# Performance work log

Hardware: AMD Instinct MI355X
Metric: run time of the kernel (lower is better)

Reference implementation:

```python
import jax, jax.numpy as jnp
import numpy as np

G, N, C, R, NCOMP, F = 1, 2097152, 16, 320, 48, 27


def _interp_plane(src, u, v):
    # src: (G, C, H, W). Torch grid_sample convention: u (grid x) indexes W (last dim),
    # v (grid y) indexes H. align_corners=True, bilinear, zero padding. Returns (G, N, C).
    _, _, H, W = src.shape
    x = (u + 1.0) * 0.5 * (W - 1)
    y = (v + 1.0) * 0.5 * (H - 1)
    x0 = jnp.floor(x)
    y0 = jnp.floor(y)
    wx = x - x0
    wy = y - y0
    x0i = x0.astype(jnp.int32)
    y0i = y0.astype(jnp.int32)

    def corner(xi, yi, w):
        inb = ((xi >= 0) & (xi < W) & (yi >= 0) & (yi < H)).astype(src.dtype)
        xc = jnp.clip(xi, 0, W - 1)
        yc = jnp.clip(yi, 0, H - 1)
        vals = jax.vmap(lambda s, yy, xx: s[:, yy, xx])(src, yc, xc)  # (G, C, N)
        return vals * (w * inb)[:, None, :]

    out = (corner(x0i, y0i, (1.0 - wx) * (1.0 - wy))
           + corner(x0i + 1, y0i, wx * (1.0 - wy))
           + corner(x0i, y0i + 1, (1.0 - wx) * wy)
           + corner(x0i + 1, y0i + 1, wx * wy))
    return out.transpose(0, 2, 1)  # (G, N, C)


def _interp_line(src, t):
    # src: (G, C, L), t in [-1, 1]. 1D linear interp, align_corners=True, zero padding.
    _, _, L = src.shape
    x = (t + 1.0) * 0.5 * (L - 1)
    x0 = jnp.floor(x)
    wx = x - x0
    x0i = x0.astype(jnp.int32)

    def corner(xi, w):
        inb = ((xi >= 0) & (xi < L)).astype(src.dtype)
        xc = jnp.clip(xi, 0, L - 1)
        vals = jax.vmap(lambda s, xx: s[:, xx])(src, xc)  # (G, C, N)
        return vals * (w * inb)[:, None, :]

    out = corner(x0i, 1.0 - wx) + corner(x0i + 1, wx)
    return out.transpose(0, 2, 1)  # (G, N, C)


def setup_inputs() -> dict:
    key = jax.random.key(0)
    ks = jax.random.split(key, 8)
    return {
        "points": jax.random.uniform(ks[0], (G, N, 3), jnp.float32, minval=-1.0, maxval=1.0),
        "matrix_components_xy": jax.random.normal(ks[1], (G, C, R, R), jnp.float32) * 0.1,
        "matrix_components_yz": jax.random.normal(ks[2], (G, C, R, R), jnp.float32) * 0.1,
        "matrix_components_xz": jax.random.normal(ks[3], (G, C, R, R), jnp.float32) * 0.1,
        "vector_components_x": jax.random.normal(ks[4], (G, C, R), jnp.float32) * 0.1,
        "vector_components_y": jax.random.normal(ks[5], (G, C, R), jnp.float32) * 0.1,
        "vector_components_z": jax.random.normal(ks[6], (G, C, R), jnp.float32) * 0.1,
        "basis_matrix": jax.random.normal(ks[7], (G, NCOMP, F), jnp.float32) * 0.1,
    }


def reference(points, matrix_components_xy, matrix_components_yz, matrix_components_xz,
              vector_components_x, vector_components_y, vector_components_z, basis_matrix):
    recorded_shape = points.shape
    p = points.reshape(points.shape[0], -1, points.shape[-1])  # (G, N, 3)
    px, py, pz = p[..., 0], p[..., 1], p[..., 2]
    # points[..., :2] -> grid x = px (indexes W of xy plane), grid y = py
    a = _interp_plane(matrix_components_xy, px, py) * _interp_line(vector_components_z, pz)
    # points[..., [0, 2]] -> grid x = px, grid y = pz
    b = _interp_plane(matrix_components_xz, px, pz) * _interp_line(vector_components_y, py)
    # points[..., 1:] -> grid x = py, grid y = pz
    c = _interp_plane(matrix_components_yz, py, pz) * _interp_line(vector_components_x, px)
    feats = jnp.concatenate((a, b, c), axis=-1)  # (G, N, 3C)
    result = jnp.einsum('gnc,gcf->gnf', feats, basis_matrix)  # (G, N, F)
    return result.reshape(*recorded_shape[:-1], -1)
```

## Files before the change

kernel.cpp:

```cpp
#include <hip/hip_runtime.h>
#include <hip/hip_fp16.h>
#include <stdint.h>


constexpr int NPTS = 2097152;
constexpr int CCH  = 16;
constexpr int RES  = 320;
constexpr long long HW = (long long)RES * RES;
constexpr int FD   = 27;
constexpr int BLK  = 256;
constexpr int NCELL = 512;
constexpr int PTS_PER_SORTBLK = 4096;

constexpr int HIST_BLOCKS = NPTS / PTS_PER_SORTBLK;
constexpr int PLANE_BLOCKS = 1200;
constexpr int LINE_BLOCKS = 4;

constexpr size_t WS_PLANEH = 0;
constexpr size_t WS_LINEH  = WS_PLANEH + 3ull*HW*CCH*2;
constexpr size_t WS_BFRAG  = WS_LINEH + 3ull*RES*CCH*2;
constexpr size_t WS_CHIST  = WS_BFRAG + 3072;
constexpr size_t WS_CURSOR = WS_CHIST + (size_t)NCELL*4;
constexpr size_t WS_SORTED = WS_CURSOR + (size_t)NCELL*4;
constexpr size_t WS_NEED   = WS_SORTED + (size_t)NPTS*16;

typedef _Float16 half8 __attribute__((ext_vector_type(8)));
typedef float f32x16 __attribute__((ext_vector_type(16)));

__device__ __forceinline__ unsigned spread3(unsigned v) {
    return (v & 1u) | ((v & 2u) << 2) | ((v & 4u) << 4);
}
__device__ __forceinline__ int cell_key8(float px, float py, float pz) {
    int cx = min(max((int)((px + 1.f) * 4.f), 0), 7);
    int cy = min(max((int)((py + 1.f) * 4.f), 0), 7);
    int cz = min(max((int)((pz + 1.f) * 4.f), 0), 7);
    return (int)(spread3((unsigned)cx) | (spread3((unsigned)cy) << 1) | (spread3((unsigned)cz) << 2));
}

__global__ __launch_bounds__(BLK) void prep_kernel(
    const float* __restrict__ pts,
    const float* __restrict__ pxy, const float* __restrict__ pxz, const float* __restrict__ pyz,
    const float* __restrict__ vx, const float* __restrict__ vy, const float* __restrict__ vz,
    const float* __restrict__ basis,
    __half* __restrict__ planesH, __half* __restrict__ linesH, __half* __restrict__ bfragH,
    unsigned* __restrict__ chist) {
    __shared__ unsigned lh[NCELL];
    const int bid = blockIdx.x;
    const int tid = threadIdx.x;
    if (bid < HIST_BLOCKS) {
        lh[tid] = 0u; lh[tid + 256] = 0u;
        __syncthreads();
        const float4* p4 = ((const float4*)pts) + (size_t)bid * 3072;
        #pragma unroll
        for (int g = 0; g < 4; ++g) {
            const float4 a = p4[tid*12 + g*3 + 0];
            const float4 b = p4[tid*12 + g*3 + 1];
            const float4 c = p4[tid*12 + g*3 + 2];
            atomicAdd(&lh[cell_key8(a.x, a.y, a.z)], 1u);
            atomicAdd(&lh[cell_key8(a.w, b.x, b.y)], 1u);
            atomicAdd(&lh[cell_key8(b.z, b.w, c.x)], 1u);
            atomicAdd(&lh[cell_key8(c.y, c.z, c.w)], 1u);
        }
        __syncthreads();
        if (lh[tid])       atomicAdd(&chist[tid],       lh[tid]);
        if (lh[tid + 256]) atomicAdd(&chist[tid + 256], lh[tid + 256]);
    } else if (bid < HIST_BLOCKS + PLANE_BLOCKS) {
        const int pb = bid - HIST_BLOCKS;
        const int plane = pb / 400;
        const int texel = (pb % 400) * BLK + tid;
        const float* src = (plane == 0) ? pxy : (plane == 1 ? pxz : pyz);
        union { ushort u[16]; uint4 q[2]; } pk;
        #pragma unroll
        for (int c = 0; c < CCH; ++c)
            pk.u[c] = __half_as_ushort(__float2half(src[(size_t)c * HW + texel]));
        uint4* dst = (uint4*)(planesH + ((size_t)plane * HW + texel) * CCH);
        dst[0] = pk.q[0]; dst[1] = pk.q[1];
    } else if (bid < HIST_BLOCKS + PLANE_BLOCKS + LINE_BLOCKS) {
        const int idx = (bid - HIST_BLOCKS - PLANE_BLOCKS) * BLK + tid;
        if (idx >= 3 * RES) return;
        const int axis = idx / RES, t = idx % RES;
        const float* src = (axis == 0) ? vx : (axis == 1 ? vy : vz);
        union { ushort u[16]; uint4 q[2]; } pk;
        #pragma unroll
        for (int c = 0; c < CCH; ++c)
            pk.u[c] = __half_as_ushort(__float2half(src[c * RES + t]));
        uint4* dst = (uint4*)(linesH + ((size_t)axis * RES + t) * CCH);
        dst[0] = pk.q[0]; dst[1] = pk.q[1];
    } else {
        if (tid < 192) {
            const int r = tid >> 6, l = tid & 63;
            const int col = l & 31, kb = l >> 5;
            __half* dst = bfragH + tid * 8;
            #pragma unroll
            for (int j = 0; j < 8; ++j) {
                float v = (col < FD) ? basis[(r * 16 + kb * 8 + j) * FD + col] : 0.f;
                dst[j] = __float2half(v);
            }
        }
    }
}

__global__ __launch_bounds__(NCELL) void scan_kernel(const unsigned* __restrict__ chist,
                                                     unsigned* __restrict__ cursor) {
    __shared__ unsigned l[NCELL];
    const int t = threadIdx.x;
    const unsigned v = chist[t];
    l[t] = v;
    __syncthreads();
    for (int o = 1; o < NCELL; o <<= 1) {
        unsigned u = (t >= o) ? l[t - o] : 0u;
        __syncthreads();
        l[t] += u;
        __syncthreads();
    }
    cursor[t] = l[t] - v;
}

__global__ __launch_bounds__(BLK) void scatter_kernel(const float* __restrict__ pts,
                                                      unsigned* __restrict__ cursor,
                                                      float4* __restrict__ sorted) {
    __shared__ unsigned lh[NCELL];
    __shared__ unsigned lb[NCELL];
    const int bid = blockIdx.x;
    const int tid = threadIdx.x;
    lh[tid] = 0u; lh[tid + 256] = 0u;
    __syncthreads();
    const float4* p4 = ((const float4*)pts) + (size_t)bid * 3072;
    unsigned kr[16];
    #pragma unroll
    for (int g = 0; g < 4; ++g) {
        const float4 a = p4[tid*12 + g*3 + 0];
        const float4 b = p4[tid*12 + g*3 + 1];
        const float4 c = p4[tid*12 + g*3 + 2];
        int k; unsigned r;
        k = cell_key8(a.x, a.y, a.z); r = atomicAdd(&lh[k], 1u); kr[g*4+0] = ((unsigned)k << 16) | r;
        k = cell_key8(a.w, b.x, b.y); r = atomicAdd(&lh[k], 1u); kr[g*4+1] = ((unsigned)k << 16) | r;
        k = cell_key8(b.z, b.w, c.x); r = atomicAdd(&lh[k], 1u); kr[g*4+2] = ((unsigned)k << 16) | r;
        k = cell_key8(c.y, c.z, c.w); r = atomicAdd(&lh[k], 1u); kr[g*4+3] = ((unsigned)k << 16) | r;
    }
    __syncthreads();
    lb[tid]       = atomicAdd(&cursor[tid],       lh[tid]);
    lb[tid + 256] = atomicAdd(&cursor[tid + 256], lh[tid + 256]);
    __syncthreads();
    const int ibase = bid * PTS_PER_SORTBLK + tid * 16;
    #pragma unroll
    for (int g = 0; g < 4; ++g) {
        const float4 a = p4[tid*12 + g*3 + 0];
        const float4 b = p4[tid*12 + g*3 + 1];
        const float4 c = p4[tid*12 + g*3 + 2];
        unsigned e;
        e = kr[g*4+0]; sorted[lb[e >> 16] + (e & 0xffffu)] = make_float4(a.x, a.y, a.z, __int_as_float(ibase + g*4 + 0));
        e = kr[g*4+1]; sorted[lb[e >> 16] + (e & 0xffffu)] = make_float4(a.w, b.x, b.y, __int_as_float(ibase + g*4 + 1));
        e = kr[g*4+2]; sorted[lb[e >> 16] + (e & 0xffffu)] = make_float4(b.z, b.w, c.x, __int_as_float(ibase + g*4 + 2));
        e = kr[g*4+3]; sorted[lb[e >> 16] + (e & 0xffffu)] = make_float4(c.y, c.z, c.w, __int_as_float(ibase + g*4 + 3));
    }
}

__device__ __forceinline__ half8 interp8h(const uint4* __restrict__ P, const uint4* __restrict__ L,
                                          int t00, int t01, int t10, int t11, int l0, int l1,
                                          float wc, float wr, float lw, int h) {
    union U { uint4 u; __half2 h2[4]; half8 v; };
    U c00, c01, c10, c11, la, lb, res;
    c00.u = P[2*t00 + h]; c01.u = P[2*t01 + h];
    c10.u = P[2*t10 + h]; c11.u = P[2*t11 + h];
    la.u  = L[2*l0 + h];  lb.u  = L[2*l1 + h];
    const float w00 = (1.f - wc) * (1.f - wr), w01 = wc * (1.f - wr);
    const float w10 = (1.f - wc) * wr,         w11 = wc * wr;
    const __half2 w00h = __float2half2_rn(w00), w01h = __float2half2_rn(w01);
    const __half2 w10h = __float2half2_rn(w10), w11h = __float2half2_rn(w11);
    const __half2 lwh  = __float2half2_rn(lw),  mlwh = __float2half2_rn(1.f - lw);
    #pragma unroll
    for (int q = 0; q < 4; ++q) {
        __half2 s = __hmul2(c00.h2[q], w00h);
        s = __hfma2(c01.h2[q], w01h, s);
        s = __hfma2(c10.h2[q], w10h, s);
        s = __hfma2(c11.h2[q], w11h, s);
        __half2 l = __hmul2(la.h2[q], mlwh);
        l = __hfma2(lb.h2[q], lwh, l);
        res.h2[q] = __hmul2(s, l);
    }
    return res.v;
}

__global__ __launch_bounds__(BLK) void eval_kernel(
    const float4* __restrict__ sorted,
    const __half* __restrict__ planesH,
    const __half* __restrict__ linesH,
    const __half* __restrict__ bfragH,
    float* __restrict__ out) {
    __shared__ int s_oi[BLK];
    constexpr int NBLK = NPTS / BLK;
    constexpr int CHUNK = NBLK / 8;
    const int bid = blockIdx.x;
    const int tid = threadIdx.x;
    const int swz = (bid & 7) * CHUNK + (bid >> 3);
    const int wid = tid >> 6, lane = tid & 63;
    const int pcol = lane & 31, kb = lane >> 5;

    union BU { uint4 u; half8 h; } b0u, b1u, b2u;
    const uint4* bf = (const uint4*)bfragH;
    b0u.u = bf[lane]; b1u.u = bf[64 + lane]; b2u.u = bf[128 + lane];

    const uint4* Pxy = (const uint4*)planesH;
    const uint4* Pxz = (const uint4*)(planesH + (size_t)HW * CCH);
    const uint4* Pyz = (const uint4*)(planesH + (size_t)2 * HW * CCH);
    const uint4* Lx = (const uint4*)linesH;
    const uint4* Ly = (const uint4*)(linesH + (size_t)RES * CCH);
    const uint4* Lz = (const uint4*)(linesH + (size_t)2 * RES * CCH);

    const int blockbase = swz * BLK;
    #pragma unroll
    for (int t = 0; t < 2; ++t) {
        const int tbase = wid * 64 + t * 32;
        const float4 pt = sorted[blockbase + tbase + pcol];
        const float px = pt.x, py = pt.y, pz = pt.z;
        if (kb == 0) s_oi[tbase + pcol] = __float_as_int(pt.w);

        const float scl = 0.5f * (RES - 1);
        const float fx = (px + 1.f) * scl, fy = (py + 1.f) * scl, fz = (pz + 1.f) * scl;
        const float xf = floorf(fx), yf = floorf(fy), zf = floorf(fz);
        const float wx = fx - xf, wy = fy - yf, wz = fz - zf;
        int x0 = min(max((int)xf, 0), RES - 1);
        int y0 = min(max((int)yf, 0), RES - 1);
        int z0 = min(max((int)zf, 0), RES - 1);
        const int x1 = min(x0 + 1, RES - 1);
        const int y1 = min(y0 + 1, RES - 1);
        const int z1 = min(z0 + 1, RES - 1);

        f32x16 acc;
        #pragma unroll
        for (int r = 0; r < 16; ++r) acc[r] = 0.f;

        half8 a0 = interp8h(Pxy, Lz, y0*RES+x0, y0*RES+x1, y1*RES+x0, y1*RES+x1, z0, z1, wx, wy, wz, kb);
        acc = __builtin_amdgcn_mfma_f32_32x32x16_f16(a0, b0u.h, acc, 0, 0, 0);
        half8 a1 = interp8h(Pxz, Ly, z0*RES+x0, z0*RES+x1, z1*RES+x0, z1*RES+x1, y0, y1, wx, wz, wy, kb);
        acc = __builtin_amdgcn_mfma_f32_32x32x16_f16(a1, b1u.h, acc, 0, 0, 0);
        half8 a2 = interp8h(Pyz, Lx, z0*RES+y0, z0*RES+y1, z1*RES+y0, z1*RES+y1, x0, x1, wy, wz, wx, kb);
        acc = __builtin_amdgcn_mfma_f32_32x32x16_f16(a2, b2u.h, acc, 0, 0, 0);

        if (pcol < FD) {
            #pragma unroll
            for (int r = 0; r < 16; ++r) {
                const int row = (r & 3) + 8 * (r >> 2) + 4 * kb;
                const int o = s_oi[tbase + row];
                out[(size_t)o * FD + pcol] = acc[r];
            }
        }
    }
}

__device__ __forceinline__ float bilerp(const float* __restrict__ p,
                                        int o00, int o01, int o10, int o11,
                                        float wc, float wr) {
    float v00 = p[o00], v01 = p[o01], v10 = p[o10], v11 = p[o11];
    float top = v00 + wc * (v01 - v00);
    float bot = v10 + wc * (v11 - v10);
    return top + wr * (bot - top);
}

__global__ __launch_bounds__(BLK) void vm_eval_fallback(
    const float* __restrict__ pts,
    const float* __restrict__ pxy, const float* __restrict__ pyz, const float* __restrict__ pxz,
    const float* __restrict__ vx, const float* __restrict__ vy, const float* __restrict__ vz,
    const float* __restrict__ basis, float* __restrict__ out) {
    const long long i = (long long)blockIdx.x * BLK + threadIdx.x;
    const float px = pts[i*3], py = pts[i*3+1], pz = pts[i*3+2];
    const float scl = 0.5f * (RES - 1);
    const float fx = (px + 1.f) * scl, fy = (py + 1.f) * scl, fz = (pz + 1.f) * scl;
    const float xf = floorf(fx), yf = floorf(fy), zf = floorf(fz);
    const float wx = fx - xf, wy = fy - yf, wz = fz - zf;
    int x0 = min(max((int)xf, 0), RES - 1);
    int y0 = min(max((int)yf, 0), RES - 1);
    int z0 = min(max((int)zf, 0), RES - 1);
    const int x1 = min(x0+1, RES-1), y1 = min(y0+1, RES-1), z1 = min(z0+1, RES-1);
    float acc[FD];
    #pragma unroll
    for (int f = 0; f < FD; ++f) acc[f] = 0.f;
    #pragma unroll 4
    for (int c = 0; c < CCH; ++c) {
        const float* a = pxy + c * HW;
        const float* b = pxz + c * HW;
        const float* d = pyz + c * HW;
        float lz = vz[c*RES+z0]; lz += wz * (vz[c*RES+z1] - lz);
        float ly = vy[c*RES+y0]; ly += wy * (vy[c*RES+y1] - ly);
        float lx = vx[c*RES+x0]; lx += wx * (vx[c*RES+x1] - lx);
        const float fa = bilerp(a, y0*RES+x0, y0*RES+x1, y1*RES+x0, y1*RES+x1, wx, wy) * lz;
        const float fb = bilerp(b, z0*RES+x0, z0*RES+x1, z1*RES+x0, z1*RES+x1, wx, wz) * ly;
        const float fc = bilerp(d, z0*RES+y0, z0*RES+y1, z1*RES+y0, z1*RES+y1, wy, wz) * lx;
        #pragma unroll
        for (int f = 0; f < FD; ++f)
            acc[f] += fa * basis[c*FD+f] + fb * basis[(CCH+c)*FD+f] + fc * basis[(2*CCH+c)*FD+f];
    }
    float* op = out + i * FD;
    #pragma unroll
    for (int f = 0; f < FD; ++f) op[f] = acc[f];
}

extern "C" void kernel_launch(void* const* d_in, const int* in_sizes, int n_in,
                              void* d_out, int out_size, void* d_ws, size_t ws_size,
                              hipStream_t stream) {
    const float* pts   = (const float*)d_in[0];
    const float* pxy   = (const float*)d_in[1];
    const float* pyz   = (const float*)d_in[2];
    const float* pxz   = (const float*)d_in[3];
    const float* vx    = (const float*)d_in[4];
    const float* vy    = (const float*)d_in[5];
    const float* vz    = (const float*)d_in[6];
    const float* basis = (const float*)d_in[7];
    float* out = (float*)d_out;

    if (ws_size < WS_NEED) {
        vm_eval_fallback<<<NPTS / BLK, BLK, 0, stream>>>(pts, pxy, pyz, pxz, vx, vy, vz, basis, out);
        return;
    }

    uint8_t* w = (uint8_t*)d_ws;
    __half*   planesH = (__half*)(w + WS_PLANEH);
    __half*   linesH  = (__half*)(w + WS_LINEH);
    __half*   bfragH  = (__half*)(w + WS_BFRAG);
    unsigned* chist   = (unsigned*)(w + WS_CHIST);
    unsigned* cursor  = (unsigned*)(w + WS_CURSOR);
    float4*   sorted  = (float4*)(w + WS_SORTED);

    hipMemsetAsync(chist, 0, (size_t)NCELL * 4, stream);
    prep_kernel<<<HIST_BLOCKS + PLANE_BLOCKS + LINE_BLOCKS + 1, BLK, 0, stream>>>(
        pts, pxy, pxz, pyz, vx, vy, vz, basis, planesH, linesH, bfragH, chist);
    scan_kernel<<<1, NCELL, 0, stream>>>(chist, cursor);
    scatter_kernel<<<HIST_BLOCKS, BLK, 0, stream>>>(pts, cursor, sorted);
    eval_kernel<<<NPTS / BLK, BLK, 0, stream>>>(sorted, planesH, linesH, bfragH, out);
}
```

Measured before the change: 200.5 us.

## Bin points into 16^3 cells and interpolate from per-cell LDS texture patches

```diff
diff --git a/kernel.cpp b/kernel.cpp
--- a/kernel.cpp
+++ b/kernel.cpp
@@ -9,10 +9,15 @@
 constexpr long long HW = (long long)RES * RES;
 constexpr int FD   = 27;
 constexpr int BLK  = 256;
-constexpr int NCELL = 512;
-constexpr int PTS_PER_SORTBLK = 4096;
-
-constexpr int HIST_BLOCKS = NPTS / PTS_PER_SORTBLK;
+constexpr int CDIM = 16;
+constexpr int NCELL = CDIM * CDIM * CDIM;
+constexpr int PATCH = 22;
+constexpr int PP_U4 = PATCH * PATCH * 2;
+constexpr int PL_U4 = 3 * PP_U4;
+constexpr int LN_U4 = 3 * PATCH * 2;
+constexpr int SORT_BLOCKS = 64;
+constexpr int PTS_PER_SORT = NPTS / SORT_BLOCKS;
+
 constexpr int PLANE_BLOCKS = 1200;
 constexpr int LINE_BLOCKS = 4;
 
@@ -27,14 +32,11 @@
 typedef _Float16 half8 __attribute__((ext_vector_type(8)));
 typedef float f32x16 __attribute__((ext_vector_type(16)));
 
-__device__ __forceinline__ unsigned spread3(unsigned v) {
-    return (v & 1u) | ((v & 2u) << 2) | ((v & 4u) << 4);
-}
-__device__ __forceinline__ int cell_key8(float px, float py, float pz) {
-    int cx = min(max((int)((px + 1.f) * 4.f), 0), 7);
-    int cy = min(max((int)((py + 1.f) * 4.f), 0), 7);
-    int cz = min(max((int)((pz + 1.f) * 4.f), 0), 7);
-    return (int)(spread3((unsigned)cx) | (spread3((unsigned)cy) << 1) | (spread3((unsigned)cz) << 2));
+__device__ __forceinline__ int cell_key16(float px, float py, float pz) {
+    int cx = min(max((int)((px + 1.f) * 8.f), 0), 15);
+    int cy = min(max((int)((py + 1.f) * 8.f), 0), 15);
+    int cz = min(max((int)((pz + 1.f) * 8.f), 0), 15);
+    return (cz << 8) | (cy << 4) | cx;
 }
 
 __global__ __launch_bounds__(BLK) void prep_kernel(
@@ -47,25 +49,27 @@
     __shared__ unsigned lh[NCELL];
     const int bid = blockIdx.x;
     const int tid = threadIdx.x;
-    if (bid < HIST_BLOCKS) {
-        lh[tid] = 0u; lh[tid + 256] = 0u;
+    if (bid < SORT_BLOCKS) {
+        #pragma unroll
+        for (int k = 0; k < NCELL / BLK; ++k) lh[tid + k * BLK] = 0u;
         __syncthreads();
-        const float4* p4 = ((const float4*)pts) + (size_t)bid * 3072;
-        #pragma unroll
-        for (int g = 0; g < 4; ++g) {
-            const float4 a = p4[tid*12 + g*3 + 0];
-            const float4 b = p4[tid*12 + g*3 + 1];
-            const float4 c = p4[tid*12 + g*3 + 2];
-            atomicAdd(&lh[cell_key8(a.x, a.y, a.z)], 1u);
-            atomicAdd(&lh[cell_key8(a.w, b.x, b.y)], 1u);
-            atomicAdd(&lh[cell_key8(b.z, b.w, c.x)], 1u);
-            atomicAdd(&lh[cell_key8(c.y, c.z, c.w)], 1u);
+        const float4* p4 = ((const float4*)pts) + (size_t)bid * (PTS_PER_SORT * 3 / 4);
+        for (int g = 0; g < 32; ++g) {
+            const int t = g * BLK + tid;
+            const float4 a = p4[t*3+0], b = p4[t*3+1], c = p4[t*3+2];
+            atomicAdd(&lh[cell_key16(a.x, a.y, a.z)], 1u);
+            atomicAdd(&lh[cell_key16(a.w, b.x, b.y)], 1u);
+            atomicAdd(&lh[cell_key16(b.z, b.w, c.x)], 1u);
+            atomicAdd(&lh[cell_key16(c.y, c.z, c.w)], 1u);
         }
         __syncthreads();
-        if (lh[tid])       atomicAdd(&chist[tid],       lh[tid]);
-        if (lh[tid + 256]) atomicAdd(&chist[tid + 256], lh[tid + 256]);
-    } else if (bid < HIST_BLOCKS + PLANE_BLOCKS) {
-        const int pb = bid - HIST_BLOCKS;
+        #pragma unroll
+        for (int k = 0; k < NCELL / BLK; ++k) {
+            const int i = tid + k * BLK;
+            if (lh[i]) atomicAdd(&chist[i], lh[i]);
+        }
+    } else if (bid < SORT_BLOCKS + PLANE_BLOCKS) {
+        const int pb = bid - SORT_BLOCKS;
         const int plane = pb / 400;
         const int texel = (pb % 400) * BLK + tid;
         const float* src = (plane == 0) ? pxy : (plane == 1 ? pxz : pyz);
@@ -75,8 +79,8 @@
             pk.u[c] = __half_as_ushort(__float2half(src[(size_t)c * HW + texel]));
         uint4* dst = (uint4*)(planesH + ((size_t)plane * HW + texel) * CCH);
         dst[0] = pk.q[0]; dst[1] = pk.q[1];
-    } else if (bid < HIST_BLOCKS + PLANE_BLOCKS + LINE_BLOCKS) {
-        const int idx = (bid - HIST_BLOCKS - PLANE_BLOCKS) * BLK + tid;
+    } else if (bid < SORT_BLOCKS + PLANE_BLOCKS + LINE_BLOCKS) {
+        const int idx = (bid - SORT_BLOCKS - PLANE_BLOCKS) * BLK + tid;
         if (idx >= 3 * RES) return;
         const int axis = idx / RES, t = idx % RES;
         const float* src = (axis == 0) ? vx : (axis == 1 ? vy : vz);
@@ -100,70 +104,77 @@
     }
 }
 
-__global__ __launch_bounds__(NCELL) void scan_kernel(const unsigned* __restrict__ chist,
-                                                     unsigned* __restrict__ cursor) {
-    __shared__ unsigned l[NCELL];
+__global__ __launch_bounds__(1024) void scan_kernel(const unsigned* __restrict__ chist,
+                                                    unsigned* __restrict__ cursor) {
+    __shared__ unsigned lsum[1024];
     const int t = threadIdx.x;
-    const unsigned v = chist[t];
-    l[t] = v;
-    __syncthreads();
-    for (int o = 1; o < NCELL; o <<= 1) {
-        unsigned u = (t >= o) ? l[t - o] : 0u;
+    const uint4 v = ((const uint4*)chist)[t];
+    const unsigned run = v.x + v.y + v.z + v.w;
+    lsum[t] = run;
+    __syncthreads();
+    for (int o = 1; o < 1024; o <<= 1) {
+        unsigned u = (t >= o) ? lsum[t - o] : 0u;
         __syncthreads();
-        l[t] += u;
+        lsum[t] += u;
         __syncthreads();
     }
-    cursor[t] = l[t] - v;
+    const unsigned b = lsum[t] - run;
+    ((uint4*)cursor)[t] = make_uint4(b, b + v.x, b + v.x + v.y, b + v.x + v.y + v.z);
 }
 
 __global__ __launch_bounds__(BLK) void scatter_kernel(const float* __restrict__ pts,
                                                       unsigned* __restrict__ cursor,
                                                       float4* __restrict__ sorted) {
     __shared__ unsigned lh[NCELL];
+    __shared__ unsigned lh2[NCELL];
     __shared__ unsigned lb[NCELL];
     const int bid = blockIdx.x;
     const int tid = threadIdx.x;
-    lh[tid] = 0u; lh[tid + 256] = 0u;
-    __syncthreads();
-    const float4* p4 = ((const float4*)pts) + (size_t)bid * 3072;
-    unsigned kr[16];
-    #pragma unroll
-    for (int g = 0; g < 4; ++g) {
-        const float4 a = p4[tid*12 + g*3 + 0];
-        const float4 b = p4[tid*12 + g*3 + 1];
-        const float4 c = p4[tid*12 + g*3 + 2];
+    #pragma unroll
+    for (int k = 0; k < NCELL / BLK; ++k) { lh[tid + k*BLK] = 0u; lh2[tid + k*BLK] = 0u; }
+    __syncthreads();
+    const float4* p4 = ((const float4*)pts) + (size_t)bid * (PTS_PER_SORT * 3 / 4);
+    for (int g = 0; g < 32; ++g) {
+        const int t = g * BLK + tid;
+        const float4 a = p4[t*3+0], b = p4[t*3+1], c = p4[t*3+2];
+        atomicAdd(&lh[cell_key16(a.x, a.y, a.z)], 1u);
+        atomicAdd(&lh[cell_key16(a.w, b.x, b.y)], 1u);
+        atomicAdd(&lh[cell_key16(b.z, b.w, c.x)], 1u);
+        atomicAdd(&lh[cell_key16(c.y, c.z, c.w)], 1u);
+    }
+    __syncthreads();
+    #pragma unroll
+    for (int k = 0; k < NCELL / BLK; ++k) {
+        const int i = tid + k * BLK;
+        lb[i] = lh[i] ? atomicAdd(&cursor[i], lh[i]) : 0u;
+    }
+    __syncthreads();
+    const int ibase = bid * PTS_PER_SORT;
+    for (int g = 0; g < 32; ++g) {
+        const int t = g * BLK + tid;
+        const float4 a = p4[t*3+0], b = p4[t*3+1], c = p4[t*3+2];
+        const int i0 = ibase + t * 4;
         int k; unsigned r;
-        k = cell_key8(a.x, a.y, a.z); r = atomicAdd(&lh[k], 1u); kr[g*4+0] = ((unsigned)k << 16) | r;
-        k = cell_key8(a.w, b.x, b.y); r = atomicAdd(&lh[k], 1u); kr[g*4+1] = ((unsigned)k << 16) | r;
-        k = cell_key8(b.z, b.w, c.x); r = atomicAdd(&lh[k], 1u); kr[g*4+2] = ((unsigned)k << 16) | r;
-        k = cell_key8(c.y, c.z, c.w); r = atomicAdd(&lh[k], 1u); kr[g*4+3] = ((unsigned)k << 16) | r;
-    }
-    __syncthreads();
-    lb[tid]       = atomicAdd(&cursor[tid],       lh[tid]);
-    lb[tid + 256] = atomicAdd(&cursor[tid + 256], lh[tid + 256]);
-    __syncthreads();
-    const int ibase = bid * PTS_PER_SORTBLK + tid * 16;
-    #pragma unroll
-    for (int g = 0; g < 4; ++g) {
-        const float4 a = p4[tid*12 + g*3 + 0];
-        const float4 b = p4[tid*12 + g*3 + 1];
-        const float4 c = p4[tid*12 + g*3 + 2];
-        unsigned e;
-        e = kr[g*4+0]; sorted[lb[e >> 16] + (e & 0xffffu)] = make_float4(a.x, a.y, a.z, __int_as_float(ibase + g*4 + 0));
-        e = kr[g*4+1]; sorted[lb[e >> 16] + (e & 0xffffu)] = make_float4(a.w, b.x, b.y, __int_as_float(ibase + g*4 + 1));
-        e = kr[g*4+2]; sorted[lb[e >> 16] + (e & 0xffffu)] = make_float4(b.z, b.w, c.x, __int_as_float(ibase + g*4 + 2));
-        e = kr[g*4+3]; sorted[lb[e >> 16] + (e & 0xffffu)] = make_float4(c.y, c.z, c.w, __int_as_float(ibase + g*4 + 3));
-    }
-}
-
-__device__ __forceinline__ half8 interp8h(const uint4* __restrict__ P, const uint4* __restrict__ L,
-                                          int t00, int t01, int t10, int t11, int l0, int l1,
-                                          float wc, float wr, float lw, int h) {
+        k = cell_key16(a.x, a.y, a.z); r = atomicAdd(&lh2[k], 1u);
+        sorted[lb[k] + r] = make_float4(a.x, a.y, a.z, __int_as_float(i0 + 0));
+        k = cell_key16(a.w, b.x, b.y); r = atomicAdd(&lh2[k], 1u);
+        sorted[lb[k] + r] = make_float4(a.w, b.x, b.y, __int_as_float(i0 + 1));
+        k = cell_key16(b.z, b.w, c.x); r = atomicAdd(&lh2[k], 1u);
+        sorted[lb[k] + r] = make_float4(b.z, b.w, c.x, __int_as_float(i0 + 2));
+        k = cell_key16(c.y, c.z, c.w); r = atomicAdd(&lh2[k], 1u);
+        sorted[lb[k] + r] = make_float4(c.y, c.z, c.w, __int_as_float(i0 + 3));
+    }
+}
+
+__device__ __forceinline__ half8 interp8_lds(const uint4* __restrict__ sp,
+                                             int i00, int i01, int i10, int i11,
+                                             int il0, int il1,
+                                             float wc, float wr, float lw) {
     union U { uint4 u; __half2 h2[4]; half8 v; };
     U c00, c01, c10, c11, la, lb, res;
-    c00.u = P[2*t00 + h]; c01.u = P[2*t01 + h];
-    c10.u = P[2*t10 + h]; c11.u = P[2*t11 + h];
-    la.u  = L[2*l0 + h];  lb.u  = L[2*l1 + h];
+    c00.u = sp[i00]; c01.u = sp[i01];
+    c10.u = sp[i10]; c11.u = sp[i11];
+    la.u  = sp[il0]; lb.u  = sp[il1];
     const float w00 = (1.f - wc) * (1.f - wr), w01 = wc * (1.f - wr);
     const float w10 = (1.f - wc) * wr,         w11 = wc * wr;
     const __half2 w00h = __float2half2_rn(w00), w01h = __float2half2_rn(w01);
@@ -187,63 +198,98 @@
     const __half* __restrict__ planesH,
     const __half* __restrict__ linesH,
     const __half* __restrict__ bfragH,
+    const unsigned* __restrict__ chist,
+    const unsigned* __restrict__ cursor,
     float* __restrict__ out) {
+    __shared__ uint4 s_patch[PL_U4 + LN_U4];
     __shared__ int s_oi[BLK];
-    constexpr int NBLK = NPTS / BLK;
-    constexpr int CHUNK = NBLK / 8;
     const int bid = blockIdx.x;
     const int tid = threadIdx.x;
-    const int swz = (bid & 7) * CHUNK + (bid >> 3);
+    const int cell = (bid & 7) * (NCELL / 8) + (bid >> 3);
+    const int cx = cell & 15, cy = (cell >> 4) & 15, cz = cell >> 8;
+    const int bx = (cx * 319) >> 4, by = (cy * 319) >> 4, bz = (cz * 319) >> 4;
+
+    for (int i = tid; i < PL_U4; i += BLK) {
+        const int p = i / PP_U4, rem = i - p * PP_U4;
+        const int r = rem / 44, c4 = rem - r * 44;
+        const int tx = c4 >> 1, h = c4 & 1;
+        const int rb = (p == 0) ? by : bz;
+        const int cb = (p == 2) ? by : bx;
+        const int gr = min(rb + r, RES - 1), gc = min(cb + tx, RES - 1);
+        s_patch[i] = ((const uint4*)(planesH + ((size_t)p * HW + (size_t)gr * RES + gc) * CCH))[h];
+    }
+    for (int i = tid; i < LN_U4; i += BLK) {
+        const int a = i / 44, rem = i - a * 44;
+        const int t = rem >> 1, h = rem & 1;
+        const int ab = (a == 0) ? bx : (a == 1) ? by : bz;
+        const int gt = min(ab + t, RES - 1);
+        s_patch[PL_U4 + i] = ((const uint4*)(linesH + ((size_t)a * RES + gt) * CCH))[h];
+    }
+
     const int wid = tid >> 6, lane = tid & 63;
     const int pcol = lane & 31, kb = lane >> 5;
-
     union BU { uint4 u; half8 h; } b0u, b1u, b2u;
     const uint4* bf = (const uint4*)bfragH;
     b0u.u = bf[lane]; b1u.u = bf[64 + lane]; b2u.u = bf[128 + lane];
 
-    const uint4* Pxy = (const uint4*)planesH;
-    const uint4* Pxz = (const uint4*)(planesH + (size_t)HW * CCH);
-    const uint4* Pyz = (const uint4*)(planesH + (size_t)2 * HW * CCH);
-    const uint4* Lx = (const uint4*)linesH;
-    const uint4* Ly = (const uint4*)(linesH + (size_t)RES * CCH);
-    const uint4* Lz = (const uint4*)(linesH + (size_t)2 * RES * CCH);
-
-    const int blockbase = swz * BLK;
-    #pragma unroll
-    for (int t = 0; t < 2; ++t) {
-        const int tbase = wid * 64 + t * 32;
-        const float4 pt = sorted[blockbase + tbase + pcol];
-        const float px = pt.x, py = pt.y, pz = pt.z;
-        if (kb == 0) s_oi[tbase + pcol] = __float_as_int(pt.w);
-
-        const float scl = 0.5f * (RES - 1);
-        const float fx = (px + 1.f) * scl, fy = (py + 1.f) * scl, fz = (pz + 1.f) * scl;
-        const float xf = floorf(fx), yf = floorf(fy), zf = floorf(fz);
-        const float wx = fx - xf, wy = fy - yf, wz = fz - zf;
-        int x0 = min(max((int)xf, 0), RES - 1);
-        int y0 = min(max((int)yf, 0), RES - 1);
-        int z0 = min(max((int)zf, 0), RES - 1);
-        const int x1 = min(x0 + 1, RES - 1);
-        const int y1 = min(y0 + 1, RES - 1);
-        const int z1 = min(z0 + 1, RES - 1);
-
-        f32x16 acc;
-        #pragma unroll
-        for (int r = 0; r < 16; ++r) acc[r] = 0.f;
-
-        half8 a0 = interp8h(Pxy, Lz, y0*RES+x0, y0*RES+x1, y1*RES+x0, y1*RES+x1, z0, z1, wx, wy, wz, kb);
-        acc = __builtin_amdgcn_mfma_f32_32x32x16_f16(a0, b0u.h, acc, 0, 0, 0);
-        half8 a1 = interp8h(Pxz, Ly, z0*RES+x0, z0*RES+x1, z1*RES+x0, z1*RES+x1, y0, y1, wx, wz, wy, kb);
-        acc = __builtin_amdgcn_mfma_f32_32x32x16_f16(a1, b1u.h, acc, 0, 0, 0);
-        half8 a2 = interp8h(Pyz, Lx, z0*RES+y0, z0*RES+y1, z1*RES+y0, z1*RES+y1, x0, x1, wy, wz, wx, kb);
-        acc = __builtin_amdgcn_mfma_f32_32x32x16_f16(a2, b2u.h, acc, 0, 0, 0);
-
-        if (pcol < FD) {
-            #pragma unroll
-            for (int r = 0; r < 16; ++r) {
-                const int row = (r & 3) + 8 * (r >> 2) + 4 * kb;
-                const int o = s_oi[tbase + row];
-                out[(size_t)o * FD + pcol] = acc[r];
+    __syncthreads();
+
+    const int cnt = (int)chist[cell];
+    const int start = (int)cursor[cell] - cnt;
+
+    for (int base = 0; base < cnt; base += BLK) {
+        #pragma unroll
+        for (int t = 0; t < 2; ++t) {
+            const int tb = wid * 64 + t * 32;
+            if (base + tb < cnt) {
+                const int slot = base + tb + pcol;
+                const float4 pt = sorted[start + min(slot, cnt - 1)];
+                if (kb == 0) s_oi[tb + pcol] = __float_as_int(pt.w);
+
+                const float scl = 0.5f * (RES - 1);
+                const float fx = (pt.x + 1.f) * scl, fy = (pt.y + 1.f) * scl, fz = (pt.z + 1.f) * scl;
+                const float xf = floorf(fx), yf = floorf(fy), zf = floorf(fz);
+                const float wx = fx - xf, wy = fy - yf, wz = fz - zf;
+                int x0 = min(max((int)xf, 0), RES - 1);
+                int y0 = min(max((int)yf, 0), RES - 1);
+                int z0 = min(max((int)zf, 0), RES - 1);
+                const int x1 = min(x0 + 1, RES - 1);
+                const int y1 = min(y0 + 1, RES - 1);
+                const int z1 = min(z0 + 1, RES - 1);
+                const int lx0 = x0 - bx, lx1 = x1 - bx;
+                const int ly0 = y0 - by, ly1 = y1 - by;
+                const int lz0 = z0 - bz, lz1 = z1 - bz;
+
+                f32x16 acc;
+                #pragma unroll
+                for (int r = 0; r < 16; ++r) acc[r] = 0.f;
+
+                half8 a0 = interp8_lds(s_patch,
+                    (ly0*PATCH + lx0)*2 + kb, (ly0*PATCH + lx1)*2 + kb,
+                    (ly1*PATCH + lx0)*2 + kb, (ly1*PATCH + lx1)*2 + kb,
+                    PL_U4 + 2*44 + lz0*2 + kb, PL_U4 + 2*44 + lz1*2 + kb, wx, wy, wz);
+                acc = __builtin_amdgcn_mfma_f32_32x32x16_f16(a0, b0u.h, acc, 0, 0, 0);
+                half8 a1 = interp8_lds(s_patch,
+                    PP_U4 + (lz0*PATCH + lx0)*2 + kb, PP_U4 + (lz0*PATCH + lx1)*2 + kb,
+                    PP_U4 + (lz1*PATCH + lx0)*2 + kb, PP_U4 + (lz1*PATCH + lx1)*2 + kb,
+                    PL_U4 + 1*44 + ly0*2 + kb, PL_U4 + 1*44 + ly1*2 + kb, wx, wz, wy);
+                acc = __builtin_amdgcn_mfma_f32_32x32x16_f16(a1, b1u.h, acc, 0, 0, 0);
+                half8 a2 = interp8_lds(s_patch,
+                    2*PP_U4 + (lz0*PATCH + ly0)*2 + kb, 2*PP_U4 + (lz0*PATCH + ly1)*2 + kb,
+                    2*PP_U4 + (lz1*PATCH + ly0)*2 + kb, 2*PP_U4 + (lz1*PATCH + ly1)*2 + kb,
+                    PL_U4 + 0*44 + lx0*2 + kb, PL_U4 + 0*44 + lx1*2 + kb, wy, wz, wx);
+                acc = __builtin_amdgcn_mfma_f32_32x32x16_f16(a2, b2u.h, acc, 0, 0, 0);
+
+                if (pcol < FD) {
+                    #pragma unroll
+                    for (int r = 0; r < 16; ++r) {
+                        const int row = (r & 3) + 8 * (r >> 2) + 4 * kb;
+                        if (base + tb + row < cnt) {
+                            const int o = s_oi[tb + row];
+                            out[(size_t)o * FD + pcol] = acc[r];
+                        }
+                    }
+                }
             }
         }
     }
@@ -323,9 +369,9 @@
     float4*   sorted  = (float4*)(w + WS_SORTED);
 
     hipMemsetAsync(chist, 0, (size_t)NCELL * 4, stream);
-    prep_kernel<<<HIST_BLOCKS + PLANE_BLOCKS + LINE_BLOCKS + 1, BLK, 0, stream>>>(
+    prep_kernel<<<SORT_BLOCKS + PLANE_BLOCKS + LINE_BLOCKS + 1, BLK, 0, stream>>>(
         pts, pxy, pxz, pyz, vx, vy, vz, basis, planesH, linesH, bfragH, chist);
-    scan_kernel<<<1, NCELL, 0, stream>>>(chist, cursor);
-    scatter_kernel<<<HIST_BLOCKS, BLK, 0, stream>>>(pts, cursor, sorted);
-    eval_kernel<<<NPTS / BLK, BLK, 0, stream>>>(sorted, planesH, linesH, bfragH, out);
-}
+    scan_kernel<<<1, 1024, 0, stream>>>(chist, cursor);
+    scatter_kernel<<<SORT_BLOCKS, BLK, 0, stream>>>(pts, cursor, sorted);
+    eval_kernel<<<NCELL, BLK, 0, stream>>>(sorted, planesH, linesH, bfragH, chist, cursor, out);
+}
```

Result: slower. 223.6 us (+11.5%).
